# Optimization experiments

Hardware: AMD Instinct MI355X
Metric: run time of the kernel (lower is better)

Reference implementation:

```python
import jax, jax.numpy as jnp
import numpy as np

EMB = 512
HEADS = 8
HEAD_DIM = EMB // HEADS


def setup_inputs() -> dict:
    key = jax.random.key(0)
    ks = jax.random.split(key, 9)
    s = 1.0 / np.sqrt(EMB)
    return {
        "x": jax.random.normal(ks[0], (4, 2048, EMB), dtype=jnp.float32),
        "Wq": jax.random.uniform(ks[1], (EMB, EMB), jnp.float32, -s, s),
        "bq": jax.random.uniform(ks[2], (EMB,), jnp.float32, -s, s),
        "Wk": jax.random.uniform(ks[3], (EMB, EMB), jnp.float32, -s, s),
        "bk": jax.random.uniform(ks[4], (EMB,), jnp.float32, -s, s),
        "Wv": jax.random.uniform(ks[5], (EMB, EMB), jnp.float32, -s, s),
        "bv": jax.random.uniform(ks[6], (EMB,), jnp.float32, -s, s),
        "Wp": jax.random.uniform(ks[7], (EMB, EMB), jnp.float32, -s, s),
        "bp": jax.random.uniform(ks[8], (EMB,), jnp.float32, -s, s),
    }


def _split_heads(t):
    b, n, _ = t.shape
    return t.reshape(b, n, HEADS, HEAD_DIM).transpose(0, 2, 1, 3)  # b h n d


def reference(x, Wq, bq, Wk, bk, Wv, bv, Wp, bp):
    q = _split_heads(x @ Wq.T + bq)
    k = _split_heads(x @ Wk.T + bk)
    v = _split_heads(x @ Wv.T + bv)
    energy = jnp.einsum("bhqd,bhkd->bhqk", q, k)
    # NOTE: original applies softmax to UNSCALED logits, then divides probs by sqrt(emb)
    att = jax.nn.softmax(energy, axis=-1) / jnp.sqrt(jnp.float32(EMB))
    out = jnp.einsum("bhqk,bhkd->bhqd", att, v)
    b, h, n, d = out.shape
    out = out.transpose(0, 2, 1, 3).reshape(b, n, h * d)
    return out @ Wp.T + bp
```

## Files before the change

### kernel.cpp

```cpp
#include <hip/hip_runtime.h>
#include <math.h>
#include <stdint.h>

#define SEQ  2048
#define NH   8
#define HD   64
#define MTOT 8192
#define LOG2E 1.4426950408889634f

typedef __attribute__((ext_vector_type(4))) float f32x4;
typedef __attribute__((ext_vector_type(16))) float f32x16;
typedef __attribute__((ext_vector_type(8))) short bf16x8;

__device__ __forceinline__ unsigned short bfu(float f) {
    return (unsigned short)((__float_as_uint(f) + 0x8000u) >> 16);
}
__device__ __forceinline__ unsigned packbf(float a, float b) {
    return __builtin_amdgcn_perm(__float_as_uint(b) + 0x8000u,
                                 __float_as_uint(a) + 0x8000u, 0x07060302u);
}

__device__ __forceinline__ void gl_lds16(const void* g, const void* l) {
    __builtin_amdgcn_global_load_lds(
        (const __attribute__((address_space(1))) unsigned int*)g,
        (__attribute__((address_space(3))) unsigned int*)l, 16, 0, 0);
}

__global__ __launch_bounds__(256) void convert_kernel(
    const float* __restrict__ x,  const float* __restrict__ wq,
    const float* __restrict__ wk, const float* __restrict__ wv,
    const float* __restrict__ wp, unsigned short* __restrict__ dst)
{
    const long i = ((long)blockIdx.x * 256 + threadIdx.x) * 4;
    if (i >= 5242880L) return;
    const float* src; long off;
    if      (i < 4194304L) { src = x;  off = i; }
    else if (i < 4456448L) { src = wq; off = i - 4194304L; }
    else if (i < 4718592L) { src = wk; off = i - 4456448L; }
    else if (i < 4980736L) { src = wv; off = i - 4718592L; }
    else                   { src = wp; off = i - 4980736L; }
    const float4 a = *(const float4*)(src + off);
    uint2 o;
    o.x = packbf(a.x, a.y);
    o.y = packbf(a.z, a.w);
    *(uint2*)(dst + i) = o;
}

template <int MODE, int TR>
__global__ __launch_bounds__(256, 2) void gemm_kernel(
    const unsigned short* __restrict__ A, const unsigned short* __restrict__ W,
    const float* __restrict__ b0, const float* __restrict__ b1,
    const float* __restrict__ b2,
    unsigned short* __restrict__ Qw, unsigned short* __restrict__ Kw,
    unsigned short* __restrict__ VTw, float* __restrict__ Fout)
{
    constexpr int BN = (MODE == 0) ? 128 : 64;
    constexpr int NT = BN / 32;
    constexpr int BSTR = BN * 32;
    __shared__ __align__(16) unsigned short smem[16384];
    const int t = threadIdx.x;
    const int w = t >> 6, lane = t & 63, quad = (t >> 4) & 3, l15 = t & 15;
    const int wr = w >> 1, wc = w & 1;
    const int m0 = blockIdx.y * 128;
    const int n0 = blockIdx.x * BN + ((MODE == 0 && TR == 0) ? 1024 : 0);

    f32x4 acc[4][NT];
#pragma unroll
    for (int mt = 0; mt < 4; ++mt)
#pragma unroll
        for (int nt = 0; nt < NT; ++nt) acc[mt][nt] = (f32x4){0.f, 0.f, 0.f, 0.f};

    auto stage = [&](int buf, int k0) {
#pragma unroll
        for (int i = 0; i < 2; ++i) {
            const int ci = w * 2 + i;
            gl_lds16(A + (size_t)(m0 + ci * 16 + l15) * 512 + k0 + quad * 8,
                     smem + buf * 4096 + ci * 512);
            if (MODE == 0)
                gl_lds16(W + (size_t)(n0 + ci * 16 + l15) * 512 + k0 + quad * 8,
                         smem + 8192 + buf * BSTR + ci * 512);
        }
        if (MODE == 1)
            gl_lds16(W + (size_t)(n0 + w * 16 + l15) * 512 + k0 + quad * 8,
                     smem + 8192 + buf * BSTR + w * 512);
    };

    stage(0, 0);
    __syncthreads();
    int buf = 0;
    for (int ki = 0; ki < 16; ++ki) {
        if (ki < 15) stage(buf ^ 1, (ki + 1) * 32);
        const unsigned short* As = smem + buf * 4096;
        const unsigned short* Bs = smem + 8192 + buf * BSTR;
        bf16x8 af[4], bfr[NT];
#pragma unroll
        for (int mt = 0; mt < 4; ++mt)
            af[mt] = *(const bf16x8*)(As + ((wr * 4 + mt) * 64 + lane) * 8);
#pragma unroll
        for (int nt = 0; nt < NT; ++nt)
            bfr[nt] = *(const bf16x8*)(Bs + ((wc * NT + nt) * 64 + lane) * 8);
#pragma unroll
        for (int mt = 0; mt < 4; ++mt)
#pragma unroll
            for (int nt = 0; nt < NT; ++nt) {
                if (TR)
                    acc[mt][nt] = __builtin_amdgcn_mfma_f32_16x16x32_bf16(
                        bfr[nt], af[mt], acc[mt][nt], 0, 0, 0);
                else
                    acc[mt][nt] = __builtin_amdgcn_mfma_f32_16x16x32_bf16(
                        af[mt], bfr[nt], acc[mt][nt], 0, 0, 0);
            }
        buf ^= 1;
        if (ki < 15) __syncthreads();
    }

    if (MODE == 1) {
#pragma unroll
        for (int nt = 0; nt < NT; ++nt) {
            const int n = n0 + wc * 32 + nt * 16 + l15;
            const float bias = b0[n];
#pragma unroll
            for (int mt = 0; mt < 4; ++mt) {
                const int mb = m0 + wr * 64 + mt * 16 + quad * 4;
                const f32x4 v = acc[mt][nt];
#pragma unroll
                for (int r = 0; r < 4; ++r)
                    Fout[(size_t)(mb + r) * 512 + n] = v[r] + bias;
            }
        }
    } else if (TR == 0) {
#pragma unroll
        for (int nt = 0; nt < 4; ++nt) {
            const int n = n0 + wc * 64 + nt * 16 + l15;
            const float bias = b2[n & 511];
            const int h = (n >> 6) & 7, d = n & 63;
#pragma unroll
            for (int mt = 0; mt < 4; ++mt) {
                const int mb = m0 + wr * 64 + mt * 16 + quad * 4;
                const int bi = mb >> 11, ns = mb & 2047;
                const f32x4 v = acc[mt][nt];
                unsigned short* dst =
                    VTw + ((size_t)(bi * 8 + h) * 64 + d) * SEQ + ns;
                uint2 pk;
                pk.x = packbf(v[0] + bias, v[1] + bias);
                pk.y = packbf(v[2] + bias, v[3] + bias);
                *(uint2*)dst = pk;
            }
        }
    } else {
        const int which = n0 >> 9;
        const float sc = which ? 1.f : LOG2E;
        const float* bp = which ? b1 : b0;
        unsigned short* base = which ? Kw : Qw;
#pragma unroll
        for (int nt = 0; nt < 4; ++nt) {
            const int nb = n0 + wc * 64 + nt * 16 + quad * 4;
            const f32x4 bv = *(const f32x4*)(bp + (nb & 511));
            const int h = (nb >> 6) & 7, d0 = nb & 63;
#pragma unroll
            for (int mt = 0; mt < 4; ++mt) {
                const int nsg = m0 + wr * 64 + mt * 16 + l15;
                const int bi = nsg >> 11, ns = nsg & 2047;
                const f32x4 v = acc[mt][nt];
                const float f0 = (v[0] + bv[0]) * sc, f1 = (v[1] + bv[1]) * sc;
                const float f2 = (v[2] + bv[2]) * sc, f3 = (v[3] + bv[3]) * sc;
                uint2 pk;
                pk.x = packbf(f0, f1);
                pk.y = packbf(f2, f3);
                *(uint2*)(base + ((size_t)(bi * 8 + h) * SEQ + ns) * 64 + d0) = pk;
            }
        }
    }
}

__global__ __launch_bounds__(256, 2) void attn_kernel(
    const unsigned short* __restrict__ Q, const unsigned short* __restrict__ K,
    const unsigned short* __restrict__ VT, unsigned short* __restrict__ Ow)
{
    __shared__ __align__(16) unsigned short smem[24576];
    const int t = threadIdx.x;
    const int w = t >> 6, lane = t & 63;
    const int l31 = lane & 31, hlf = lane >> 5;

    const int bh = blockIdx.x;
    const int q0 = blockIdx.y * 128;

    const unsigned short* Qb = Q + ((size_t)bh * SEQ + q0) * 64;
    const unsigned short* Kb = K + (size_t)bh * SEQ * 64;
    const unsigned short* Vb = VT + (size_t)bh * 64 * SEQ;

#pragma unroll
    for (int i = 0; i < 4; ++i)
        gl_lds16(Qb + (size_t)(w * 32 + l31) * 64 + i * 16 + hlf * 8,
                 smem + (w * 4 + i) * 512);

    auto stageKV = [&](int buf, int j0) {
#pragma unroll
        for (int i = 0; i < 2; ++i) {
            const int c = w * 2 + i;
            const int g = c >> 2, s = c & 3;
            gl_lds16(Kb + (size_t)(j0 + g * 32 + l31) * 64 + s * 16 + hlf * 8,
                     smem + 8192 + buf * 4096 + c * 512);
            gl_lds16(Vb + (size_t)(g * 32 + l31) * SEQ + j0 + s * 16 + hlf * 8,
                     smem + 16384 + buf * 4096 + c * 512);
        }
    };

    stageKV(0, 0);
    __syncthreads();

    bf16x8 qf[4];
#pragma unroll
    for (int i = 0; i < 4; ++i)
        qf[i] = *(const bf16x8*)(smem + (w * 4 + i) * 512 + lane * 8);

    f32x16 zero;
#pragma unroll
    for (int r = 0; r < 16; ++r) zero[r] = 0.f;

    float lpart = 0.f;
    f32x16 Ot[2];
    Ot[0] = zero; Ot[1] = zero;

    int buf = 0;
    for (int jt = 0; jt < 32; ++jt) {
        if (jt < 31) stageKV(buf ^ 1, (jt + 1) * 64);
        const unsigned short* Ks = smem + 8192 + buf * 4096;
        const unsigned short* Vs = smem + 16384 + buf * 4096;

        f32x16 st[2];
#pragma unroll
        for (int jg = 0; jg < 2; ++jg) {
            f32x16 c = zero;
#pragma unroll
            for (int kt = 0; kt < 4; ++kt) {
                const bf16x8 kf =
                    *(const bf16x8*)(Ks + (jg * 4 + kt) * 512 + lane * 8);
                c = __builtin_amdgcn_mfma_f32_32x32x16_bf16(kf, qf[kt], c, 0, 0, 0);
            }
            st[jg] = c;
        }

        float ls = 0.f;
#pragma unroll
        for (int jg = 0; jg < 2; ++jg)
#pragma unroll
            for (int r = 0; r < 16; ++r) {
                st[jg][r] = __builtin_amdgcn_exp2f(st[jg][r]);
                ls += st[jg][r];
            }
        lpart += ls;

        bf16x8 pf[4];
#pragma unroll
        for (int p = 0; p < 4; ++p) {
            const f32x16 c = st[p >> 1];
            const int r0 = (p & 1) * 8;
            const unsigned a0 = packbf(c[r0 + 0], c[r0 + 1]);
            const unsigned a1 = packbf(c[r0 + 2], c[r0 + 3]);
            const unsigned b0 = packbf(c[r0 + 4], c[r0 + 5]);
            const unsigned b1 = packbf(c[r0 + 6], c[r0 + 7]);
            const unsigned ta0 = (unsigned)__shfl_xor((int)a0, 32);
            const unsigned ta1 = (unsigned)__shfl_xor((int)a1, 32);
            const unsigned tb0 = (unsigned)__shfl_xor((int)b0, 32);
            const unsigned tb1 = (unsigned)__shfl_xor((int)b1, 32);
            union { unsigned u[4]; bf16x8 v; } pb;
            pb.u[0] = hlf ? tb0 : a0;
            pb.u[1] = hlf ? tb1 : a1;
            pb.u[2] = hlf ? b0 : ta0;
            pb.u[3] = hlf ? b1 : ta1;
            pf[p] = pb.v;
        }

#pragma unroll
        for (int dg = 0; dg < 2; ++dg)
#pragma unroll
            for (int p = 0; p < 4; ++p) {
                const bf16x8 vf =
                    *(const bf16x8*)(Vs + (dg * 4 + p) * 512 + lane * 8);
                Ot[dg] = __builtin_amdgcn_mfma_f32_32x32x16_bf16(
                    vf, pf[p], Ot[dg], 0, 0, 0);
            }

        buf ^= 1;
        if (jt < 31) __syncthreads();
    }

    const float lv = lpart + __shfl_xor(lpart, 32);
    const float inv = 1.0f / (lv * 22.627416997969522f);

    const int bi = bh >> 3, h = bh & 7;
    const int ns = q0 + w * 32 + l31;
    unsigned short* dst = Ow + ((size_t)bi * SEQ + ns) * 512 + h * 64 + hlf * 4;
#pragma unroll
    for (int dg = 0; dg < 2; ++dg)
#pragma unroll
        for (int rb = 0; rb < 4; ++rb) {
            uint2 pk;
            pk.x = packbf(Ot[dg][rb * 4 + 0] * inv, Ot[dg][rb * 4 + 1] * inv);
            pk.y = packbf(Ot[dg][rb * 4 + 2] * inv, Ot[dg][rb * 4 + 3] * inv);
            *(uint2*)(dst + dg * 32 + rb * 8) = pk;
        }
}

extern "C" void kernel_launch(void* const* d_in, const int* in_sizes, int n_in,
                              void* d_out, int out_size, void* d_ws, size_t ws_size,
                              hipStream_t stream)
{
    const float* x  = (const float*)d_in[0];
    const float* Wq = (const float*)d_in[1];
    const float* bq = (const float*)d_in[2];
    const float* Wk = (const float*)d_in[3];
    const float* bk = (const float*)d_in[4];
    const float* Wv = (const float*)d_in[5];
    const float* bv = (const float*)d_in[6];
    const float* Wp = (const float*)d_in[7];
    const float* bp = (const float*)d_in[8];

    unsigned short* ws = (unsigned short*)d_ws;
    unsigned short* xb    = ws;
    unsigned short* Wqkvb = ws + 4194304;
    unsigned short* Wpb   = ws + 4980736;
    unsigned short* Qw    = ws + 5242880;
    unsigned short* Kw    = Qw + 4194304;
    unsigned short* VTw   = Kw + 4194304;
    unsigned short* Owb   = VTw + 4194304;

    convert_kernel<<<5120, 256, 0, stream>>>(x, Wq, Wk, Wv, Wp, ws);
    gemm_kernel<0, 1><<<dim3(8, 64), 256, 0, stream>>>(
        xb, Wqkvb, bq, bk, bv, Qw, Kw, VTw, nullptr);
    gemm_kernel<0, 0><<<dim3(4, 64), 256, 0, stream>>>(
        xb, Wqkvb, bq, bk, bv, Qw, Kw, VTw, nullptr);
    attn_kernel<<<dim3(32, 16), 256, 0, stream>>>(Qw, Kw, VTw, Owb);
    gemm_kernel<1, 0><<<dim3(8, 64), 256, 0, stream>>>(
        Owb, Wpb, bp, nullptr, nullptr, nullptr, nullptr, nullptr, (float*)d_out);
}
```

Baseline: 184.8 us.

## Merge QKV GEMM launches and split attention KV across wave pairs

```diff
diff --git a/kernel.cpp b/kernel.cpp
--- a/kernel.cpp
+++ b/kernel.cpp
@@ -12,9 +12,8 @@
 typedef __attribute__((ext_vector_type(16))) float f32x16;
 typedef __attribute__((ext_vector_type(8))) short bf16x8;
 
-__device__ __forceinline__ unsigned short bfu(float f) {
-    return (unsigned short)((__float_as_uint(f) + 0x8000u) >> 16);
-}
+template <int V> struct IC { static constexpr int value = V; };
+
 __device__ __forceinline__ unsigned packbf(float a, float b) {
     return __builtin_amdgcn_perm(__float_as_uint(b) + 0x8000u,
                                  __float_as_uint(a) + 0x8000u, 0x07060302u);
@@ -46,8 +45,8 @@
     *(uint2*)(dst + i) = o;
 }
 
-template <int MODE, int TR>
-__global__ __launch_bounds__(256, 2) void gemm_kernel(
+template <int MODE>
+__global__ __launch_bounds__(256, MODE == 0 ? 3 : 2) void gemm_kernel(
     const unsigned short* __restrict__ A, const unsigned short* __restrict__ W,
     const float* __restrict__ b0, const float* __restrict__ b1,
     const float* __restrict__ b2,
@@ -62,7 +61,7 @@
     const int w = t >> 6, lane = t & 63, quad = (t >> 4) & 3, l15 = t & 15;
     const int wr = w >> 1, wc = w & 1;
     const int m0 = blockIdx.y * 128;
-    const int n0 = blockIdx.x * BN + ((MODE == 0 && TR == 0) ? 1024 : 0);
+    const int n0 = blockIdx.x * BN;
 
     f32x4 acc[4][NT];
 #pragma unroll
@@ -85,34 +84,40 @@
                      smem + 8192 + buf * BSTR + w * 512);
     };
 
+    int buf = 0;
     stage(0, 0);
     __syncthreads();
-    int buf = 0;
-    for (int ki = 0; ki < 16; ++ki) {
-        if (ki < 15) stage(buf ^ 1, (ki + 1) * 32);
-        const unsigned short* As = smem + buf * 4096;
-        const unsigned short* Bs = smem + 8192 + buf * BSTR;
-        bf16x8 af[4], bfr[NT];
-#pragma unroll
-        for (int mt = 0; mt < 4; ++mt)
-            af[mt] = *(const bf16x8*)(As + ((wr * 4 + mt) * 64 + lane) * 8);
-#pragma unroll
-        for (int nt = 0; nt < NT; ++nt)
-            bfr[nt] = *(const bf16x8*)(Bs + ((wc * NT + nt) * 64 + lane) * 8);
-#pragma unroll
-        for (int mt = 0; mt < 4; ++mt)
-#pragma unroll
-            for (int nt = 0; nt < NT; ++nt) {
-                if (TR)
-                    acc[mt][nt] = __builtin_amdgcn_mfma_f32_16x16x32_bf16(
-                        bfr[nt], af[mt], acc[mt][nt], 0, 0, 0);
-                else
-                    acc[mt][nt] = __builtin_amdgcn_mfma_f32_16x16x32_bf16(
-                        af[mt], bfr[nt], acc[mt][nt], 0, 0, 0);
-            }
-        buf ^= 1;
-        if (ki < 15) __syncthreads();
-    }
+
+    auto kloop = [&](auto TRC) {
+        constexpr int TR = decltype(TRC)::value;
+        for (int ki = 0; ki < 16; ++ki) {
+            if (ki < 15) stage(buf ^ 1, (ki + 1) * 32);
+            const unsigned short* As = smem + buf * 4096;
+            const unsigned short* Bs = smem + 8192 + buf * BSTR;
+            bf16x8 af[4], bfr[NT];
+#pragma unroll
+            for (int mt = 0; mt < 4; ++mt)
+                af[mt] = *(const bf16x8*)(As + ((wr * 4 + mt) * 64 + lane) * 8);
+#pragma unroll
+            for (int nt = 0; nt < NT; ++nt)
+                bfr[nt] = *(const bf16x8*)(Bs + ((wc * NT + nt) * 64 + lane) * 8);
+#pragma unroll
+            for (int mt = 0; mt < 4; ++mt)
+#pragma unroll
+                for (int nt = 0; nt < NT; ++nt) {
+                    if (TR)
+                        acc[mt][nt] = __builtin_amdgcn_mfma_f32_16x16x32_bf16(
+                            bfr[nt], af[mt], acc[mt][nt], 0, 0, 0);
+                    else
+                        acc[mt][nt] = __builtin_amdgcn_mfma_f32_16x16x32_bf16(
+                            af[mt], bfr[nt], acc[mt][nt], 0, 0, 0);
+                }
+            buf ^= 1;
+            if (ki < 15) __syncthreads();
+        }
+    };
+    if (MODE == 0 && n0 < 1024) kloop(IC<1>{});
+    else                        kloop(IC<0>{});
 
     if (MODE == 1) {
 #pragma unroll
@@ -128,7 +133,7 @@
                     Fout[(size_t)(mb + r) * 512 + n] = v[r] + bias;
             }
         }
-    } else if (TR == 0) {
+    } else if (n0 >= 1024) {
 #pragma unroll
         for (int nt = 0; nt < 4; ++nt) {
             const int n = n0 + wc * 64 + nt * 16 + l15;
@@ -181,6 +186,7 @@
     const int t = threadIdx.x;
     const int w = t >> 6, lane = t & 63;
     const int l31 = lane & 31, hlf = lane >> 5;
+    const int qh = w >> 1, jh = w & 1;
 
     const int bh = blockIdx.x;
     const int q0 = blockIdx.y * 128;
@@ -206,101 +212,145 @@
         }
     };
 
+    int buf = 0;
     stageKV(0, 0);
     __syncthreads();
 
-    bf16x8 qf[4];
-#pragma unroll
-    for (int i = 0; i < 4; ++i)
-        qf[i] = *(const bf16x8*)(smem + (w * 4 + i) * 512 + lane * 8);
+    bf16x8 qf[2][4];
+#pragma unroll
+    for (int qt = 0; qt < 2; ++qt)
+#pragma unroll
+        for (int kt = 0; kt < 4; ++kt)
+            qf[qt][kt] =
+                *(const bf16x8*)(smem + ((qh * 2 + qt) * 4 + kt) * 512 + lane * 8);
 
     f32x16 zero;
 #pragma unroll
     for (int r = 0; r < 16; ++r) zero[r] = 0.f;
 
-    float lpart = 0.f;
-    f32x16 Ot[2];
-    Ot[0] = zero; Ot[1] = zero;
-
-    int buf = 0;
+    float lpart[2] = {0.f, 0.f};
+    f32x16 Ot[2][2];
+    Ot[0][0] = zero; Ot[0][1] = zero; Ot[1][0] = zero; Ot[1][1] = zero;
+
     for (int jt = 0; jt < 32; ++jt) {
         if (jt < 31) stageKV(buf ^ 1, (jt + 1) * 64);
         const unsigned short* Ks = smem + 8192 + buf * 4096;
         const unsigned short* Vs = smem + 16384 + buf * 4096;
 
         f32x16 st[2];
-#pragma unroll
-        for (int jg = 0; jg < 2; ++jg) {
-            f32x16 c = zero;
-#pragma unroll
-            for (int kt = 0; kt < 4; ++kt) {
-                const bf16x8 kf =
-                    *(const bf16x8*)(Ks + (jg * 4 + kt) * 512 + lane * 8);
-                c = __builtin_amdgcn_mfma_f32_32x32x16_bf16(kf, qf[kt], c, 0, 0, 0);
-            }
-            st[jg] = c;
-        }
-
-        float ls = 0.f;
-#pragma unroll
-        for (int jg = 0; jg < 2; ++jg)
+        st[0] = zero; st[1] = zero;
+#pragma unroll
+        for (int kt = 0; kt < 4; ++kt) {
+            const bf16x8 kf =
+                *(const bf16x8*)(Ks + (jh * 4 + kt) * 512 + lane * 8);
+            st[0] = __builtin_amdgcn_mfma_f32_32x32x16_bf16(kf, qf[0][kt], st[0], 0, 0, 0);
+            st[1] = __builtin_amdgcn_mfma_f32_32x32x16_bf16(kf, qf[1][kt], st[1], 0, 0, 0);
+        }
+
+#pragma unroll
+        for (int qt = 0; qt < 2; ++qt) {
+            float ls = 0.f;
 #pragma unroll
             for (int r = 0; r < 16; ++r) {
-                st[jg][r] = __builtin_amdgcn_exp2f(st[jg][r]);
-                ls += st[jg][r];
-            }
-        lpart += ls;
-
-        bf16x8 pf[4];
-#pragma unroll
-        for (int p = 0; p < 4; ++p) {
-            const f32x16 c = st[p >> 1];
-            const int r0 = (p & 1) * 8;
-            const unsigned a0 = packbf(c[r0 + 0], c[r0 + 1]);
-            const unsigned a1 = packbf(c[r0 + 2], c[r0 + 3]);
-            const unsigned b0 = packbf(c[r0 + 4], c[r0 + 5]);
-            const unsigned b1 = packbf(c[r0 + 6], c[r0 + 7]);
-            const unsigned ta0 = (unsigned)__shfl_xor((int)a0, 32);
-            const unsigned ta1 = (unsigned)__shfl_xor((int)a1, 32);
-            const unsigned tb0 = (unsigned)__shfl_xor((int)b0, 32);
-            const unsigned tb1 = (unsigned)__shfl_xor((int)b1, 32);
-            union { unsigned u[4]; bf16x8 v; } pb;
-            pb.u[0] = hlf ? tb0 : a0;
-            pb.u[1] = hlf ? tb1 : a1;
-            pb.u[2] = hlf ? b0 : ta0;
-            pb.u[3] = hlf ? b1 : ta1;
-            pf[p] = pb.v;
-        }
+                st[qt][r] = __builtin_amdgcn_exp2f(st[qt][r]);
+                ls += st[qt][r];
+            }
+            lpart[qt] += ls;
+        }
+
+        bf16x8 pf[2][2];
+#pragma unroll
+        for (int qt = 0; qt < 2; ++qt)
+#pragma unroll
+            for (int p = 0; p < 2; ++p) {
+                const int r0 = p * 8;
+                const unsigned a0 = packbf(st[qt][r0 + 0], st[qt][r0 + 1]);
+                const unsigned a1 = packbf(st[qt][r0 + 2], st[qt][r0 + 3]);
+                const unsigned b0 = packbf(st[qt][r0 + 4], st[qt][r0 + 5]);
+                const unsigned b1 = packbf(st[qt][r0 + 6], st[qt][r0 + 7]);
+                const unsigned ta0 = (unsigned)__shfl_xor((int)a0, 32);
+                const unsigned ta1 = (unsigned)__shfl_xor((int)a1, 32);
+                const unsigned tb0 = (unsigned)__shfl_xor((int)b0, 32);
+                const unsigned tb1 = (unsigned)__shfl_xor((int)b1, 32);
+                union { unsigned u[4]; bf16x8 v; } pb;
+                pb.u[0] = hlf ? tb0 : a0;
+                pb.u[1] = hlf ? tb1 : a1;
+                pb.u[2] = hlf ? b0 : ta0;
+                pb.u[3] = hlf ? b1 : ta1;
+                pf[qt][p] = pb.v;
+            }
 
 #pragma unroll
         for (int dg = 0; dg < 2; ++dg)
 #pragma unroll
-            for (int p = 0; p < 4; ++p) {
-                const bf16x8 vf =
-                    *(const bf16x8*)(Vs + (dg * 4 + p) * 512 + lane * 8);
-                Ot[dg] = __builtin_amdgcn_mfma_f32_32x32x16_bf16(
-                    vf, pf[p], Ot[dg], 0, 0, 0);
+            for (int p = 0; p < 2; ++p) {
+                const bf16x8 vf = *(const bf16x8*)(
+                    Vs + (dg * 4 + jh * 2 + p) * 512 + lane * 8);
+                Ot[0][dg] = __builtin_amdgcn_mfma_f32_32x32x16_bf16(
+                    vf, pf[0][p], Ot[0][dg], 0, 0, 0);
+                Ot[1][dg] = __builtin_amdgcn_mfma_f32_32x32x16_bf16(
+                    vf, pf[1][p], Ot[1][dg], 0, 0, 0);
             }
 
         buf ^= 1;
         if (jt < 31) __syncthreads();
     }
 
-    const float lv = lpart + __shfl_xor(lpart, 32);
-    const float inv = 1.0f / (lv * 22.627416997969522f);
-
-    const int bi = bh >> 3, h = bh & 7;
-    const int ns = q0 + w * 32 + l31;
-    unsigned short* dst = Ow + ((size_t)bi * SEQ + ns) * 512 + h * 64 + hlf * 4;
-#pragma unroll
-    for (int dg = 0; dg < 2; ++dg)
-#pragma unroll
-        for (int rb = 0; rb < 4; ++rb) {
-            uint2 pk;
-            pk.x = packbf(Ot[dg][rb * 4 + 0] * inv, Ot[dg][rb * 4 + 1] * inv);
-            pk.y = packbf(Ot[dg][rb * 4 + 2] * inv, Ot[dg][rb * 4 + 3] * inv);
-            *(uint2*)(dst + dg * 32 + rb * 8) = pk;
-        }
+    float* cb = (float*)smem;
+    __syncthreads();
+    if (jh == 1) {
+#pragma unroll
+        for (int qt = 0; qt < 2; ++qt) {
+#pragma unroll
+            for (int dg = 0; dg < 2; ++dg) {
+                const int cid = (qh * 4 + qt * 2 + dg) * 4;
+#pragma unroll
+                for (int k = 0; k < 4; ++k) {
+                    float4 v = make_float4(Ot[qt][dg][k * 4 + 0], Ot[qt][dg][k * 4 + 1],
+                                           Ot[qt][dg][k * 4 + 2], Ot[qt][dg][k * 4 + 3]);
+                    *(float4*)(cb + ((cid + k) * 64 + lane) * 4) = v;
+                }
+            }
+            cb[8192 + (qh * 2 + qt) * 64 + lane] = lpart[qt];
+        }
+    }
+    __syncthreads();
+    if (jh == 0) {
+        const int bi = bh >> 3, h = bh & 7;
+#pragma unroll
+        for (int qt = 0; qt < 2; ++qt) {
+#pragma unroll
+            for (int dg = 0; dg < 2; ++dg) {
+                const int cid = (qh * 4 + qt * 2 + dg) * 4;
+#pragma unroll
+                for (int k = 0; k < 4; ++k) {
+                    const float4 v = *(const float4*)(cb + ((cid + k) * 64 + lane) * 4);
+                    Ot[qt][dg][k * 4 + 0] += v.x;
+                    Ot[qt][dg][k * 4 + 1] += v.y;
+                    Ot[qt][dg][k * 4 + 2] += v.z;
+                    Ot[qt][dg][k * 4 + 3] += v.w;
+                }
+            }
+            float lv = lpart[qt] + cb[8192 + (qh * 2 + qt) * 64 + lane];
+            lv += __shfl_xor(lv, 32);
+            const float inv = 1.0f / (lv * 22.627416997969522f);
+
+            const int ns = q0 + (qh * 2 + qt) * 32 + l31;
+            unsigned short* dst =
+                Ow + ((size_t)bi * SEQ + ns) * 512 + h * 64 + hlf * 4;
+#pragma unroll
+            for (int dg = 0; dg < 2; ++dg)
+#pragma unroll
+                for (int rb = 0; rb < 4; ++rb) {
+                    uint2 pk;
+                    pk.x = packbf(Ot[qt][dg][rb * 4 + 0] * inv,
+                                  Ot[qt][dg][rb * 4 + 1] * inv);
+                    pk.y = packbf(Ot[qt][dg][rb * 4 + 2] * inv,
+                                  Ot[qt][dg][rb * 4 + 3] * inv);
+                    *(uint2*)(dst + dg * 32 + rb * 8) = pk;
+                }
+        }
+    }
 }
 
 extern "C" void kernel_launch(void* const* d_in, const int* in_sizes, int n_in,
@@ -327,11 +377,9 @@
     unsigned short* Owb   = VTw + 4194304;
 
     convert_kernel<<<5120, 256, 0, stream>>>(x, Wq, Wk, Wv, Wp, ws);
-    gemm_kernel<0, 1><<<dim3(8, 64), 256, 0, stream>>>(
-        xb, Wqkvb, bq, bk, bv, Qw, Kw, VTw, nullptr);
-    gemm_kernel<0, 0><<<dim3(4, 64), 256, 0, stream>>>(
+    gemm_kernel<0><<<dim3(12, 64), 256, 0, stream>>>(
         xb, Wqkvb, bq, bk, bv, Qw, Kw, VTw, nullptr);
     attn_kernel<<<dim3(32, 16), 256, 0, stream>>>(Qw, Kw, VTw, Owb);
-    gemm_kernel<1, 0><<<dim3(8, 64), 256, 0, stream>>>(
+    gemm_kernel<1><<<dim3(8, 64), 256, 0, stream>>>(
         Owb, Wpb, bp, nullptr, nullptr, nullptr, nullptr, nullptr, (float*)d_out);
 }
```

New measurement: 181.8 us. About the same (-1.6%).

## Pre-swizzle Q/K/V into MFMA fragment layout and drop LDS staging in attention

Applied to the files above, without the earlier changes.

```diff
diff --git a/kernel.cpp b/kernel.cpp
--- a/kernel.cpp
+++ b/kernel.cpp
@@ -12,9 +12,8 @@
 typedef __attribute__((ext_vector_type(16))) float f32x16;
 typedef __attribute__((ext_vector_type(8))) short bf16x8;
 
-__device__ __forceinline__ unsigned short bfu(float f) {
-    return (unsigned short)((__float_as_uint(f) + 0x8000u) >> 16);
-}
+template <int V> struct IC { static constexpr int value = V; };
+
 __device__ __forceinline__ unsigned packbf(float a, float b) {
     return __builtin_amdgcn_perm(__float_as_uint(b) + 0x8000u,
                                  __float_as_uint(a) + 0x8000u, 0x07060302u);
@@ -46,8 +45,8 @@
     *(uint2*)(dst + i) = o;
 }
 
-template <int MODE, int TR>
-__global__ __launch_bounds__(256, 2) void gemm_kernel(
+template <int MODE>
+__global__ __launch_bounds__(256, MODE == 0 ? 3 : 2) void gemm_kernel(
     const unsigned short* __restrict__ A, const unsigned short* __restrict__ W,
     const float* __restrict__ b0, const float* __restrict__ b1,
     const float* __restrict__ b2,
@@ -62,7 +61,7 @@
     const int w = t >> 6, lane = t & 63, quad = (t >> 4) & 3, l15 = t & 15;
     const int wr = w >> 1, wc = w & 1;
     const int m0 = blockIdx.y * 128;
-    const int n0 = blockIdx.x * BN + ((MODE == 0 && TR == 0) ? 1024 : 0);
+    const int n0 = blockIdx.x * BN;
 
     f32x4 acc[4][NT];
 #pragma unroll
@@ -85,34 +84,40 @@
                      smem + 8192 + buf * BSTR + w * 512);
     };
 
+    int buf = 0;
     stage(0, 0);
     __syncthreads();
-    int buf = 0;
-    for (int ki = 0; ki < 16; ++ki) {
-        if (ki < 15) stage(buf ^ 1, (ki + 1) * 32);
-        const unsigned short* As = smem + buf * 4096;
-        const unsigned short* Bs = smem + 8192 + buf * BSTR;
-        bf16x8 af[4], bfr[NT];
-#pragma unroll
-        for (int mt = 0; mt < 4; ++mt)
-            af[mt] = *(const bf16x8*)(As + ((wr * 4 + mt) * 64 + lane) * 8);
-#pragma unroll
-        for (int nt = 0; nt < NT; ++nt)
-            bfr[nt] = *(const bf16x8*)(Bs + ((wc * NT + nt) * 64 + lane) * 8);
-#pragma unroll
-        for (int mt = 0; mt < 4; ++mt)
-#pragma unroll
-            for (int nt = 0; nt < NT; ++nt) {
-                if (TR)
-                    acc[mt][nt] = __builtin_amdgcn_mfma_f32_16x16x32_bf16(
-                        bfr[nt], af[mt], acc[mt][nt], 0, 0, 0);
-                else
-                    acc[mt][nt] = __builtin_amdgcn_mfma_f32_16x16x32_bf16(
-                        af[mt], bfr[nt], acc[mt][nt], 0, 0, 0);
-            }
-        buf ^= 1;
-        if (ki < 15) __syncthreads();
-    }
+
+    auto kloop = [&](auto TRC) {
+        constexpr int TR = decltype(TRC)::value;
+        for (int ki = 0; ki < 16; ++ki) {
+            if (ki < 15) stage(buf ^ 1, (ki + 1) * 32);
+            const unsigned short* As = smem + buf * 4096;
+            const unsigned short* Bs = smem + 8192 + buf * BSTR;
+            bf16x8 af[4], bfr[NT];
+#pragma unroll
+            for (int mt = 0; mt < 4; ++mt)
+                af[mt] = *(const bf16x8*)(As + ((wr * 4 + mt) * 64 + lane) * 8);
+#pragma unroll
+            for (int nt = 0; nt < NT; ++nt)
+                bfr[nt] = *(const bf16x8*)(Bs + ((wc * NT + nt) * 64 + lane) * 8);
+#pragma unroll
+            for (int mt = 0; mt < 4; ++mt)
+#pragma unroll
+                for (int nt = 0; nt < NT; ++nt) {
+                    if (TR)
+                        acc[mt][nt] = __builtin_amdgcn_mfma_f32_16x16x32_bf16(
+                            bfr[nt], af[mt], acc[mt][nt], 0, 0, 0);
+                    else
+                        acc[mt][nt] = __builtin_amdgcn_mfma_f32_16x16x32_bf16(
+                            af[mt], bfr[nt], acc[mt][nt], 0, 0, 0);
+                }
+            buf ^= 1;
+            if (ki < 15) __syncthreads();
+        }
+    };
+    if (MODE == 0 && n0 < 1024) kloop(IC<1>{});
+    else                        kloop(IC<0>{});
 
     if (MODE == 1) {
 #pragma unroll
@@ -128,7 +133,7 @@
                     Fout[(size_t)(mb + r) * 512 + n] = v[r] + bias;
             }
         }
-    } else if (TR == 0) {
+    } else if (n0 >= 1024) {
 #pragma unroll
         for (int nt = 0; nt < 4; ++nt) {
             const int n = n0 + wc * 64 + nt * 16 + l15;
@@ -138,13 +143,16 @@
             for (int mt = 0; mt < 4; ++mt) {
                 const int mb = m0 + wr * 64 + mt * 16 + quad * 4;
                 const int bi = mb >> 11, ns = mb & 2047;
+                const int bhl = bi * 8 + h;
                 const f32x4 v = acc[mt][nt];
-                unsigned short* dst =
-                    VTw + ((size_t)(bi * 8 + h) * 64 + d) * SEQ + ns;
                 uint2 pk;
                 pk.x = packbf(v[0] + bias, v[1] + bias);
                 pk.y = packbf(v[2] + bias, v[3] + bias);
-                *(uint2*)dst = pk;
+                const size_t off =
+                    ((size_t)(bhl * 32 + (ns >> 6)) * 8 + ((d >> 5) << 2) +
+                     ((ns >> 4) & 3)) * 512 +
+                    ((d & 31) << 3) + ((ns & 8) << 5) + (ns & 7);
+                *(uint2*)(VTw + off) = pk;
             }
         }
     } else {
@@ -161,58 +169,40 @@
             for (int mt = 0; mt < 4; ++mt) {
                 const int nsg = m0 + wr * 64 + mt * 16 + l15;
                 const int bi = nsg >> 11, ns = nsg & 2047;
+                const int bhl = bi * 8 + h;
                 const f32x4 v = acc[mt][nt];
-                const float f0 = (v[0] + bv[0]) * sc, f1 = (v[1] + bv[1]) * sc;
-                const float f2 = (v[2] + bv[2]) * sc, f3 = (v[3] + bv[3]) * sc;
                 uint2 pk;
-                pk.x = packbf(f0, f1);
-                pk.y = packbf(f2, f3);
-                *(uint2*)(base + ((size_t)(bi * 8 + h) * SEQ + ns) * 64 + d0) = pk;
+                pk.x = packbf((v[0] + bv[0]) * sc, (v[1] + bv[1]) * sc);
+                pk.y = packbf((v[2] + bv[2]) * sc, (v[3] + bv[3]) * sc);
+                const size_t off =
+                    ((size_t)(bhl * 64 + (ns >> 5)) * 4 + (d0 >> 4)) * 512 +
+                    ((d0 & 8) << 5) + ((ns & 31) << 3) + (d0 & 7);
+                *(uint2*)(base + off) = pk;
             }
         }
     }
 }
 
 __global__ __launch_bounds__(256, 2) void attn_kernel(
-    const unsigned short* __restrict__ Q, const unsigned short* __restrict__ K,
-    const unsigned short* __restrict__ VT, unsigned short* __restrict__ Ow)
+    const unsigned short* __restrict__ Qf, const unsigned short* __restrict__ Kf,
+    const unsigned short* __restrict__ Vf, unsigned short* __restrict__ Ow)
 {
-    __shared__ __align__(16) unsigned short smem[24576];
     const int t = threadIdx.x;
     const int w = t >> 6, lane = t & 63;
     const int l31 = lane & 31, hlf = lane >> 5;
 
     const int bh = blockIdx.x;
     const int q0 = blockIdx.y * 128;
-
-    const unsigned short* Qb = Q + ((size_t)bh * SEQ + q0) * 64;
-    const unsigned short* Kb = K + (size_t)bh * SEQ * 64;
-    const unsigned short* Vb = VT + (size_t)bh * 64 * SEQ;
-
-#pragma unroll
-    for (int i = 0; i < 4; ++i)
-        gl_lds16(Qb + (size_t)(w * 32 + l31) * 64 + i * 16 + hlf * 8,
-                 smem + (w * 4 + i) * 512);
-
-    auto stageKV = [&](int buf, int j0) {
-#pragma unroll
-        for (int i = 0; i < 2; ++i) {
-            const int c = w * 2 + i;
-            const int g = c >> 2, s = c & 3;
-            gl_lds16(Kb + (size_t)(j0 + g * 32 + l31) * 64 + s * 16 + hlf * 8,
-                     smem + 8192 + buf * 4096 + c * 512);
-            gl_lds16(Vb + (size_t)(g * 32 + l31) * SEQ + j0 + s * 16 + hlf * 8,
-                     smem + 16384 + buf * 4096 + c * 512);
-        }
-    };
-
-    stageKV(0, 0);
-    __syncthreads();
+    const int qg = (q0 >> 5) + w;
+
+    const unsigned short* Qp = Qf + ((size_t)(bh * 64 + qg) * 4) * 512 + lane * 8;
+    const unsigned short* Kp = Kf + (size_t)bh * 131072 + lane * 8;
+    const unsigned short* Vp = Vf + (size_t)bh * 131072 + lane * 8;
 
     bf16x8 qf[4];
 #pragma unroll
-    for (int i = 0; i < 4; ++i)
-        qf[i] = *(const bf16x8*)(smem + (w * 4 + i) * 512 + lane * 8);
+    for (int kt = 0; kt < 4; ++kt)
+        qf[kt] = *(const bf16x8*)(Qp + kt * 512);
 
     f32x16 zero;
 #pragma unroll
@@ -222,23 +212,28 @@
     f32x16 Ot[2];
     Ot[0] = zero; Ot[1] = zero;
 
-    int buf = 0;
+    bf16x8 kc[8];
+#pragma unroll
+    for (int c = 0; c < 8; ++c)
+        kc[c] = *(const bf16x8*)(Kp + c * 512);
+
     for (int jt = 0; jt < 32; ++jt) {
-        if (jt < 31) stageKV(buf ^ 1, (jt + 1) * 64);
-        const unsigned short* Ks = smem + 8192 + buf * 4096;
-        const unsigned short* Vs = smem + 16384 + buf * 4096;
+        bf16x8 vc[8];
+#pragma unroll
+        for (int c = 0; c < 8; ++c)
+            vc[c] = *(const bf16x8*)(Vp + jt * 4096 + c * 512);
+        const int jn = (jt < 31) ? jt + 1 : 31;
+        bf16x8 kn[8];
+#pragma unroll
+        for (int c = 0; c < 8; ++c)
+            kn[c] = *(const bf16x8*)(Kp + jn * 4096 + c * 512);
 
         f32x16 st[2];
-#pragma unroll
-        for (int jg = 0; jg < 2; ++jg) {
-            f32x16 c = zero;
-#pragma unroll
-            for (int kt = 0; kt < 4; ++kt) {
-                const bf16x8 kf =
-                    *(const bf16x8*)(Ks + (jg * 4 + kt) * 512 + lane * 8);
-                c = __builtin_amdgcn_mfma_f32_32x32x16_bf16(kf, qf[kt], c, 0, 0, 0);
-            }
-            st[jg] = c;
+        st[0] = zero; st[1] = zero;
+#pragma unroll
+        for (int kt = 0; kt < 4; ++kt) {
+            st[0] = __builtin_amdgcn_mfma_f32_32x32x16_bf16(kc[kt],     qf[kt], st[0], 0, 0, 0);
+            st[1] = __builtin_amdgcn_mfma_f32_32x32x16_bf16(kc[4 + kt], qf[kt], st[1], 0, 0, 0);
         }
 
         float ls = 0.f;
@@ -275,15 +270,12 @@
 #pragma unroll
         for (int dg = 0; dg < 2; ++dg)
 #pragma unroll
-            for (int p = 0; p < 4; ++p) {
-                const bf16x8 vf =
-                    *(const bf16x8*)(Vs + (dg * 4 + p) * 512 + lane * 8);
+            for (int p = 0; p < 4; ++p)
                 Ot[dg] = __builtin_amdgcn_mfma_f32_32x32x16_bf16(
-                    vf, pf[p], Ot[dg], 0, 0, 0);
-            }
-
-        buf ^= 1;
-        if (jt < 31) __syncthreads();
+                    vc[dg * 4 + p], pf[p], Ot[dg], 0, 0, 0);
+
+#pragma unroll
+        for (int c = 0; c < 8; ++c) kc[c] = kn[c];
     }
 
     const float lv = lpart + __shfl_xor(lpart, 32);
@@ -327,11 +319,9 @@
     unsigned short* Owb   = VTw + 4194304;
 
     convert_kernel<<<5120, 256, 0, stream>>>(x, Wq, Wk, Wv, Wp, ws);
-    gemm_kernel<0, 1><<<dim3(8, 64), 256, 0, stream>>>(
-        xb, Wqkvb, bq, bk, bv, Qw, Kw, VTw, nullptr);
-    gemm_kernel<0, 0><<<dim3(4, 64), 256, 0, stream>>>(
+    gemm_kernel<0><<<dim3(12, 64), 256, 0, stream>>>(
         xb, Wqkvb, bq, bk, bv, Qw, Kw, VTw, nullptr);
     attn_kernel<<<dim3(32, 16), 256, 0, stream>>>(Qw, Kw, VTw, Owb);
-    gemm_kernel<1, 0><<<dim3(8, 64), 256, 0, stream>>>(
+    gemm_kernel<1><<<dim3(8, 64), 256, 0, stream>>>(
         Owb, Wpb, bp, nullptr, nullptr, nullptr, nullptr, nullptr, (float*)d_out);
 }
```

Result: faster. 171.2 us (-7.3%).
